# Kernel tuning notes

Hardware: AMD Instinct MI355X
Metric: run time of the kernel (lower is better)

The kernel has to match this reference:

```python
import jax, jax.numpy as jnp
import numpy as np

B, N, XS = 32, 200000, 256
SCALE = 100.0      # generator.scale_factor (grid-units per normalized coord)
CENTER = XS / 2.0  # xmipp_origin
W0_FIRST = 30.0    # SIREN first-layer frequency
SIGMA = 1.0        # gaussianFilterImage sigma
RAD = 3            # gaussian kernel radius (size 7)


def setup_inputs() -> dict:
    key = jax.random.key(0)
    ks = jax.random.split(key, 8)
    rows = jax.random.normal(ks[0], (B, 3), jnp.float32)            # euler angles (rad)
    shifts = jax.random.normal(ks[1], (B, 2), jnp.float32)          # in-plane shifts (px)
    coords = jax.random.uniform(ks[2], (N, 3), jnp.float32, -1.0, 1.0)  # point cloud in [-1,1]^3
    fan_in = 3 * N
    # SIRENFirstLayerInitializer(scale=6.0): U(-scale/fan_in, scale/fan_in)
    W1 = jax.random.uniform(ks[3], (fan_in, 8), jnp.float32, -6.0 / fan_in, 6.0 / fan_in)
    b1 = jnp.zeros((8,), jnp.float32)
    lim = float(np.sqrt(6.0 / 8.0))
    Wh = jax.random.uniform(ks[4], (3, 8, 8), jnp.float32, -lim, lim)
    bh = jnp.zeros((3, 8), jnp.float32)
    W5 = jax.random.normal(ks[5], (8, N), jnp.float32) * 0.05
    b5 = jnp.zeros((N,), jnp.float32)
    ctf = jax.random.uniform(ks[6], (B, XS, XS // 2 + 1), jnp.float32)  # rfft2 CTF filter
    return dict(rows=rows, shifts=shifts, coords=coords, W1=W1, b1=b1,
                Wh=Wh, bh=bh, W5=W5, b5=b5, ctf=ctf)


def euler_zyz(angles):
    # ZYZ Euler rotation matrices, (B,3,3)
    a, b, g = angles[:, 0], angles[:, 1], angles[:, 2]
    def rz(t):
        c, s = jnp.cos(t), jnp.sin(t)
        z, o = jnp.zeros_like(t), jnp.ones_like(t)
        return jnp.stack([jnp.stack([c, -s, z], -1),
                          jnp.stack([s, c, z], -1),
                          jnp.stack([z, z, o], -1)], -2)
    def ry(t):
        c, s = jnp.cos(t), jnp.sin(t)
        z, o = jnp.zeros_like(t), jnp.ones_like(t)
        return jnp.stack([jnp.stack([c, z, s], -1),
                          jnp.stack([z, o, z], -1),
                          jnp.stack([-s, z, c], -1)], -2)
    return rz(a) @ ry(b) @ rz(g)


def reference(rows, shifts, coords, W1, b1, Wh, bh, W5, b5, ctf):
    # --- getRotatedGrid: rotate fixed point cloud by per-image Euler angles ---
    R = euler_zyz(rows)                                   # (B,3,3)
    crot = jnp.einsum('bij,nj->bni', R, coords)           # (B,N,3)
    # --- SIREN MLP on flattened grid (Concatenate+Flatten -> Dense(8) stack) ---
    h = jnp.sin(W0_FIRST * (crot.reshape(B, 3 * N) @ W1 + b1))  # (B,8)
    for i in range(3):
        h = jnp.sin(h @ Wh[i] + bh[i])
    delta = h @ W5 + b5                                   # (B,N) per-point intensities
    # --- scatterImgByPass: bilinear scatter of intensities into (B,XS,XS) ---
    pos = crot[:, :, :2] * SCALE + CENTER - shifts[:, None, :]   # (B,N,2) -> (x,y) px
    x, y = pos[..., 0], pos[..., 1]
    x0 = jnp.floor(x); y0 = jnp.floor(y)
    fx = x - x0; fy = y - y0
    x0i = x0.astype(jnp.int32); y0i = y0.astype(jnp.int32)
    img = jnp.zeros((B, XS, XS), jnp.float32)
    bidx = jnp.arange(B, dtype=jnp.int32)[:, None]
    corners = ((0, 0, (1 - fx) * (1 - fy)), (1, 0, fx * (1 - fy)),
               (0, 1, (1 - fx) * fy), (1, 1, fx * fy))
    for dx, dy, w in corners:
        xi = x0i + dx; yi = y0i + dy
        valid = (xi >= 0) & (xi < XS) & (yi >= 0) & (yi < XS)
        xi = jnp.clip(xi, 0, XS - 1); yi = jnp.clip(yi, 0, XS - 1)
        img = img.at[bidx, yi, xi].add(jnp.where(valid, w * delta, 0.0))
    # --- gaussianFilterImage: separable gaussian blur, sigma=1 ---
    k = jnp.exp(-0.5 * (jnp.arange(-RAD, RAD + 1, dtype=jnp.float32) / SIGMA) ** 2)
    k = k / k.sum()
    dn = ('NCHW', 'OIHW', 'NCHW')
    x4 = img[:, None]                                     # (B,1,XS,XS)
    x4 = jax.lax.conv_general_dilated(x4, k.reshape(1, 1, 2 * RAD + 1, 1),
                                      (1, 1), 'SAME', dimension_numbers=dn)
    x4 = jax.lax.conv_general_dilated(x4, k.reshape(1, 1, 1, 2 * RAD + 1),
                                      (1, 1), 'SAME', dimension_numbers=dn)
    img = x4[:, 0]
    # --- ctfFilterImage: multiply by CTF in Fourier space ---
    F = jnp.fft.rfft2(img)
    out = jnp.fft.irfft2(F * ctf, s=(XS, XS))
    return out.astype(jnp.float32)
```

## Files before the change

kernel.cpp:

```cpp
#include <hip/hip_runtime.h>
#include <math.h>

constexpr int B_  = 32;
constexpr int N_  = 200000;
constexpr int XSZ = 256;
constexpr int PADS = 257;

constexpr int NQ = 4;
constexpr int BQ = 8;
constexpr int NSLAB = 32;
constexpr int BINS_Q = BQ * NSLAB;
constexpr int FILLB = 256;
constexpr int PPB = 782;
constexpr unsigned ENT_N = 1600000;

constexpr float FP_SCALE = 4194304.f;
constexpr float FP_INV   = 1.f / 4194304.f;

constexpr size_t OFF_PART  = 0;
constexpr size_t OFF_H     = 73728;
constexpr size_t OFF_R     = 74752;
constexpr size_t OFF_CNT   = 76800;
constexpr size_t OFF_INTRA = OFF_CNT + 524288;
constexpr size_t OFF_TOT   = OFF_INTRA + 1048576;
constexpr size_t OFF_BB    = OFF_TOT + 4096;
constexpr size_t OFF_APR   = OFF_BB + 4096;
constexpr size_t OFF_IMG   = OFF_APR + 1048576;
constexpr size_t OFF_ENT   = OFF_IMG + 8388608;
constexpr size_t OFF_TMP   = OFF_ENT;
constexpr size_t OFF_FC    = OFF_ENT;

__device__ __forceinline__ int rev8(int x) { return (int)(__brev((unsigned)x) >> 24); }

__device__ __forceinline__ void projPxPy(float c0, float c1, float c2,
                                         const float* sRb, const float* ssb,
                                         float& px, float& py) {
  px = fmaf(sRb[0], c0, fmaf(sRb[1], c1, fmaf(sRb[2], c2, ssb[0])));
  py = fmaf(sRb[3], c0, fmaf(sRb[4], c1, fmaf(sRb[5], c2, ssb[1])));
}

__global__ __launch_bounds__(256) void k_reduceT(const float* __restrict__ coords,
                                                 const float* __restrict__ W1,
                                                 float* __restrict__ partial) {
  float acc[72];
  #pragma unroll
  for (int t = 0; t < 72; ++t) acc[t] = 0.f;
  int idx = blockIdx.x * 256 + threadIdx.x;
  for (int n = idx; n < N_; n += 256 * 256) {
    float c0 = coords[n * 3 + 0], c1 = coords[n * 3 + 1], c2 = coords[n * 3 + 2];
    const float4* w4 = reinterpret_cast<const float4*>(W1 + (size_t)n * 24);
    #pragma unroll
    for (int i = 0; i < 3; ++i) {
      float4 wa = w4[i * 2 + 0], wb = w4[i * 2 + 1];
      float wv[8] = {wa.x, wa.y, wa.z, wa.w, wb.x, wb.y, wb.z, wb.w};
      #pragma unroll
      for (int k = 0; k < 8; ++k) {
        acc[i * 8 + k]      += c0 * wv[k];
        acc[24 + i * 8 + k] += c1 * wv[k];
        acc[48 + i * 8 + k] += c2 * wv[k];
      }
    }
  }
  #pragma unroll
  for (int t = 0; t < 72; ++t) {
    float v = acc[t];
    for (int off = 32; off > 0; off >>= 1) v += __shfl_down(v, off, 64);
    acc[t] = v;
  }
  __shared__ float sred[4][72];
  int lane = threadIdx.x & 63, wv_ = threadIdx.x >> 6;
  if (lane == 0) {
    #pragma unroll
    for (int t = 0; t < 72; ++t) sred[wv_][t] = acc[t];
  }
  __syncthreads();
  if (threadIdx.x < 72) {
    int t = threadIdx.x;
    partial[blockIdx.x * 72 + t] = sred[0][t] + sred[1][t] + sred[2][t] + sred[3][t];
  }
}

__global__ __launch_bounds__(128) void k_batch(const float* __restrict__ partial,
                                               const float* __restrict__ rows,
                                               const float* __restrict__ b1,
                                               const float* __restrict__ Wh,
                                               const float* __restrict__ bh,
                                               float* __restrict__ hbuf,
                                               float* __restrict__ Rbuf) {
  __shared__ float T[72];
  int tid = threadIdx.x;
  if (tid < 72) {
    double s = 0.0;
    for (int i = 0; i < 256; ++i) s += (double)partial[i * 72 + tid];
    T[tid] = (float)s;
  }
  __syncthreads();
  if (tid < B_) {
    int b = tid;
    float al = rows[b * 3 + 0], be = rows[b * 3 + 1], ga = rows[b * 3 + 2];
    float sa, ca, sb, cb, sg, cg;
    sincosf(al, &sa, &ca); sincosf(be, &sb, &cb); sincosf(ga, &sg, &cg);
    float R[3][3];
    R[0][0] = ca * cb * cg - sa * sg; R[0][1] = -ca * cb * sg - sa * cg; R[0][2] = ca * sb;
    R[1][0] = sa * cb * cg + ca * sg; R[1][1] = -sa * cb * sg + ca * cg; R[1][2] = sa * sb;
    R[2][0] = -sb * cg;               R[2][1] = sb * sg;                 R[2][2] = cb;
    float h[8];
    #pragma unroll
    for (int k = 0; k < 8; ++k) {
      float z = b1[k];
      #pragma unroll
      for (int i = 0; i < 3; ++i)
        #pragma unroll
        for (int j = 0; j < 3; ++j)
          z += R[i][j] * T[(j * 3 + i) * 8 + k];
      h[k] = sinf(30.f * z);
    }
    for (int l = 0; l < 3; ++l) {
      float nh[8];
      #pragma unroll
      for (int k2 = 0; k2 < 8; ++k2) {
        float z = bh[l * 8 + k2];
        #pragma unroll
        for (int k1 = 0; k1 < 8; ++k1) z += h[k1] * Wh[l * 64 + k1 * 8 + k2];
        nh[k2] = sinf(z);
      }
      #pragma unroll
      for (int k = 0; k < 8; ++k) h[k] = nh[k];
    }
    #pragma unroll
    for (int k = 0; k < 8; ++k) hbuf[b * 8 + k] = h[k];
    #pragma unroll
    for (int i = 0; i < 3; ++i)
      #pragma unroll
      for (int j = 0; j < 3; ++j) Rbuf[b * 9 + i * 3 + j] = R[i][j];
  }
}

__global__ __launch_bounds__(512) void k_count(const float* __restrict__ coords,
                                               const float* __restrict__ Rbuf,
                                               const float* __restrict__ shifts,
                                               unsigned short* __restrict__ cnt) {
  __shared__ float sR[BQ][6];
  __shared__ float ss[BQ][2];
  __shared__ unsigned hist[BINS_Q];
  int tid = threadIdx.x;
  int q = blockIdx.x >> 8;
  int fb = blockIdx.x & 255;
  if (tid < BQ) {
    int b = q * BQ + tid;
    sR[tid][0] = Rbuf[b * 9 + 0] * 100.f; sR[tid][1] = Rbuf[b * 9 + 1] * 100.f; sR[tid][2] = Rbuf[b * 9 + 2] * 100.f;
    sR[tid][3] = Rbuf[b * 9 + 3] * 100.f; sR[tid][4] = Rbuf[b * 9 + 4] * 100.f; sR[tid][5] = Rbuf[b * 9 + 5] * 100.f;
    ss[tid][0] = 128.f - shifts[b * 2 + 0];
    ss[tid][1] = 128.f - shifts[b * 2 + 1];
  }
  if (tid < BINS_Q) hist[tid] = 0;
  __syncthreads();
  int pbase = fb * PPB;
  #pragma unroll
  for (int k = 0; k < 2; ++k) {
    int off = tid + (k << 9);
    int n = pbase + off;
    if (off < PPB && n < N_) {
      float c0 = coords[n * 3], c1 = coords[n * 3 + 1], c2 = coords[n * 3 + 2];
      #pragma unroll
      for (int b = 0; b < BQ; ++b) {
        float px, py;
        projPxPy(c0, c1, c2, sR[b], ss[b], px, py);
        if (px >= -1.f && px < 256.f && py >= -1.f && py < 256.f) {
          int y0 = (int)floorf(py);
          int slab = (y0 < 0 ? 0 : y0) >> 3;
          atomicAdd(&hist[b * NSLAB + slab], 1u);
        }
      }
    }
  }
  __syncthreads();
  if (tid < BINS_Q) cnt[(size_t)blockIdx.x * BINS_Q + tid] = (unsigned short)hist[tid];
}

__global__ __launch_bounds__(256) void k_offA(const unsigned short* __restrict__ cnt,
                                              unsigned* __restrict__ intra,
                                              unsigned* __restrict__ totals) {
  int q = blockIdx.x >> 8;
  int bin = blockIdx.x & 255;
  int t = threadIdx.x;
  size_t cbase = ((size_t)q * FILLB + t) * BINS_Q + bin;
  unsigned orig = cnt[cbase];
  unsigned v = orig;
  int lane = t & 63, wid = t >> 6;
  #pragma unroll
  for (int d = 1; d < 64; d <<= 1) { unsigned u = __shfl_up(v, d, 64); if (lane >= d) v += u; }
  __shared__ unsigned wsum[4];
  if (lane == 63) wsum[wid] = v;
  __syncthreads();
  unsigned woff = 0;
  #pragma unroll
  for (int w = 0; w < 4; ++w) if (w < wid) woff += wsum[w];
  intra[cbase] = woff + v - orig;
  if (t == 255) totals[q * BINS_Q + bin] = woff + v;
}

__global__ __launch_bounds__(256) void k_offB(const unsigned* __restrict__ totals,
                                              unsigned* __restrict__ binBase) {
  int q = blockIdx.x;
  int t = threadIdx.x;
  unsigned orig = totals[q * BINS_Q + t];
  unsigned v = orig;
  int lane = t & 63, wid = t >> 6;
  #pragma unroll
  for (int d = 1; d < 64; d <<= 1) { unsigned u = __shfl_up(v, d, 64); if (lane >= d) v += u; }
  __shared__ unsigned wsum[4];
  if (lane == 63) wsum[wid] = v;
  __syncthreads();
  unsigned woff = 0;
  #pragma unroll
  for (int w = 0; w < 4; ++w) if (w < wid) woff += wsum[w];
  binBase[q * BINS_Q + t] = woff + v - orig;
}

__global__ __launch_bounds__(512) void k_fill2(const float* __restrict__ coords,
                                               const float* __restrict__ W5,
                                               const float* __restrict__ b5,
                                               const float* __restrict__ hbuf,
                                               const float* __restrict__ Rbuf,
                                               const float* __restrict__ shifts,
                                               const unsigned* __restrict__ intra,
                                               const unsigned* __restrict__ binBase,
                                               float2* __restrict__ ent) {
  __shared__ float sR[BQ][6];
  __shared__ float ss[BQ][2];
  __shared__ float sh[BQ][8];
  __shared__ unsigned scur[BINS_Q];
  int tid = threadIdx.x;
  int q = blockIdx.x >> 8;
  int fb = blockIdx.x & 255;
  if (tid < BQ) {
    int b = q * BQ + tid;
    sR[tid][0] = Rbuf[b * 9 + 0] * 100.f; sR[tid][1] = Rbuf[b * 9 + 1] * 100.f; sR[tid][2] = Rbuf[b * 9 + 2] * 100.f;
    sR[tid][3] = Rbuf[b * 9 + 3] * 100.f; sR[tid][4] = Rbuf[b * 9 + 4] * 100.f; sR[tid][5] = Rbuf[b * 9 + 5] * 100.f;
    ss[tid][0] = 128.f - shifts[b * 2 + 0];
    ss[tid][1] = 128.f - shifts[b * 2 + 1];
    #pragma unroll
    for (int k = 0; k < 8; ++k) sh[tid][k] = hbuf[b * 8 + k];
  }
  if (tid < BINS_Q)
    scur[tid] = binBase[q * BINS_Q + tid] + intra[((size_t)q * FILLB + fb) * BINS_Q + tid];
  __syncthreads();
  float2* entq = ent + (size_t)q * ENT_N;
  int pbase = fb * PPB;
  #pragma unroll
  for (int k = 0; k < 2; ++k) {
    int off = tid + (k << 9);
    int n = pbase + off;
    if (off < PPB && n < N_) {
      float c0 = coords[n * 3], c1 = coords[n * 3 + 1], c2 = coords[n * 3 + 2];
      float b5n = b5[n];
      float w5v[8];
      #pragma unroll
      for (int kk = 0; kk < 8; ++kk) w5v[kk] = W5[(size_t)kk * N_ + n];
      #pragma unroll
      for (int b = 0; b < BQ; ++b) {
        float px, py;
        projPxPy(c0, c1, c2, sR[b], ss[b], px, py);
        if (px >= -1.f && px < 256.f && py >= -1.f && py < 256.f) {
          int y0 = (int)floorf(py);
          int slab = (y0 < 0 ? 0 : y0) >> 3;
          int bin = b * NSLAB + slab;
          unsigned slot = atomicAdd(&scur[bin], 1u);
          if (slot < ENT_N) {
            float delta = b5n;
            #pragma unroll
            for (int kk = 0; kk < 8; ++kk) delta = fmaf(sh[b][kk], w5v[kk], delta);
            entq[slot] = make_float2(__int_as_float(n), delta);
          }
        }
      }
    }
  }
}

__global__ __launch_bounds__(512) void k_scatter2(const float2* __restrict__ ent,
                                                  const float* __restrict__ coords,
                                                  const float* __restrict__ Rbuf,
                                                  const float* __restrict__ shifts,
                                                  const unsigned* __restrict__ binBase,
                                                  const unsigned* __restrict__ totals,
                                                  float* __restrict__ img,
                                                  float* __restrict__ apron) {
  __shared__ int tile[9 * XSZ];
  __shared__ float sA[8];
  int tid = threadIdx.x;
  int q = blockIdx.x >> 8;
  int bin = blockIdx.x & 255;
  int b_local = bin >> 5;
  int s = bin & 31;
  int b_global = q * BQ + b_local;
  if (tid < 6)      sA[tid] = Rbuf[b_global * 9 + tid] * 100.f;
  else if (tid < 8) sA[tid] = 128.f - shifts[b_global * 2 + (tid - 6)];
  for (int i = tid; i < 9 * XSZ; i += 512) tile[i] = 0;
  __syncthreads();
  unsigned base = binBase[q * BINS_Q + bin];
  unsigned cntv = totals[q * BINS_Q + bin];
  if (base >= ENT_N) cntv = 0;
  else if (base + cntv > ENT_N) cntv = ENT_N - base;
  const float2* entq = ent + (size_t)q * ENT_N;
  int ybase = s << 3;
  for (unsigned i = tid; i < cntv; i += 512) {
    float2 e = entq[base + i];
    int n = __float_as_int(e.x);
    float delta = e.y;
    float c0 = coords[n * 3], c1 = coords[n * 3 + 1], c2 = coords[n * 3 + 2];
    float px, py;
    projPxPy(c0, c1, c2, sA, sA + 6, px, py);
    float x0f = floorf(px), y0f = floorf(py);
    float fx = px - x0f, fy = py - y0f;
    int x0 = (int)x0f;
    int r0 = (int)y0f - ybase;
    float wy0 = (1.f - fy) * delta * FP_SCALE;
    float wy1 = fy * delta * FP_SCALE;
    bool xl = (x0 >= 0), xr = (x0 <= 254);
    if (r0 >= 0) {
      int c0i = r0 * XSZ + x0;
      if (xl) atomicAdd(&tile[c0i], __float2int_rn((1.f - fx) * wy0));
      if (xr) atomicAdd(&tile[c0i + 1], __float2int_rn(fx * wy0));
    }
    int c1i = (r0 + 1) * XSZ + x0;
    if (xl) atomicAdd(&tile[c1i], __float2int_rn((1.f - fx) * wy1));
    if (xr) atomicAdd(&tile[c1i + 1], __float2int_rn(fx * wy1));
  }
  __syncthreads();
  float* imbase = img + (size_t)b_global * 65536 + (size_t)ybase * XSZ;
  for (int i = tid; i < 8 * XSZ; i += 512) imbase[i] = (float)tile[i] * FP_INV;
  if (tid < XSZ) apron[(size_t)(q * BINS_Q + bin) * XSZ + tid] = (float)tile[8 * XSZ + tid] * FP_INV;
}

__global__ __launch_bounds__(256) void k_apron(const float* __restrict__ apron,
                                               float* __restrict__ img) {
  int bid = blockIdx.x;
  int s = bid & 31;
  if (s == 31) return;
  int b = bid >> 5;
  int q = b >> 3, b_local = b & 7;
  int bin = b_local * NSLAB + s;
  int row = (s + 1) << 3;
  float* dst = img + (size_t)b * 65536 + (size_t)row * XSZ;
  dst[threadIdx.x] += apron[(size_t)(q * BINS_Q + bin) * XSZ + threadIdx.x];
}

__device__ __forceinline__ float bwv(int i) {
  const float bw[7] = {0.004433048f, 0.054005582f, 0.242036226f, 0.399050280f,
                       0.242036226f, 0.054005582f, 0.004433048f};
  return bw[i];
}

__global__ __launch_bounds__(256) void k_blurV(const float* __restrict__ in, float* __restrict__ out) {
  int i = blockIdx.x * 256 + threadIdx.x;
  int x = i & 255;
  int y = (i >> 8) & 255;
  const float* p = in + (i & ~65535);
  float s = 0.f;
  #pragma unroll
  for (int d = -3; d <= 3; ++d) {
    int yy = y + d;
    if ((unsigned)yy < XSZ) s += bwv(d + 3) * p[(yy << 8) + x];
  }
  out[i] = s;
}

__global__ __launch_bounds__(256) void k_blurH(const float* __restrict__ in, float* __restrict__ out) {
  int i = blockIdx.x * 256 + threadIdx.x;
  int x = i & 255;
  float s = 0.f;
  #pragma unroll
  for (int d = -3; d <= 3; ++d) {
    int xx = x + d;
    if ((unsigned)xx < XSZ) s += bwv(d + 3) * in[i + d];
  }
  out[i] = s;
}

__device__ __forceinline__ void fft_dif_fwd(float* re, float* im, const float2* tw, int P, int tid) {
  for (int s = 7; s >= 0; --s) {
    __syncthreads();
    int half = 1 << s;
    for (int q = tid; q < (P << 7); q += 256) {
      int p = q >> 7, k = q & 127;
      int j = k & (half - 1);
      int i0 = ((k >> s) << (s + 1)) | j;
      int i1 = i0 + half;
      float* rp = re + p * PADS; float* ip = im + p * PADS;
      float ar = rp[i0], ai = ip[i0], br = rp[i1], bi = ip[i1];
      rp[i0] = ar + br; ip[i0] = ai + bi;
      float tr = ar - br, ti = ai - bi;
      float2 w = tw[j << (7 - s)];
      rp[i1] = tr * w.x - ti * w.y;
      ip[i1] = tr * w.y + ti * w.x;
    }
  }
  __syncthreads();
}

__device__ __forceinline__ void fft_dit_inv(float* re, float* im, const float2* tw, int P, int tid) {
  for (int s = 0; s <= 7; ++s) {
    __syncthreads();
    int half = 1 << s;
    for (int q = tid; q < (P << 7); q += 256) {
      int p = q >> 7, k = q & 127;
      int j = k & (half - 1);
      int i0 = ((k >> s) << (s + 1)) | j;
      int i1 = i0 + half;
      float* rp = re + p * PADS; float* ip = im + p * PADS;
      float2 w = tw[j << (7 - s)];
      float br = rp[i1], bi = ip[i1];
      float tr = br * w.x + bi * w.y;
      float ti = bi * w.x - br * w.y;
      float ar = rp[i0], ai = ip[i0];
      rp[i0] = ar + tr; ip[i0] = ai + ti;
      rp[i1] = ar - tr; ip[i1] = ai - ti;
    }
  }
  __syncthreads();
}

__device__ __forceinline__ void tw_init(float2* tw, int tid) {
  for (int k = tid; k < 128; k += 256) {
    float s_, c_;
    sincosf(-6.2831853071795864769f * (float)k / 256.0f, &s_, &c_);
    tw[k] = make_float2(c_, s_);
  }
}

__global__ __launch_bounds__(256) void k_fft1(const float* __restrict__ img, float2* __restrict__ Fc) {
  __shared__ float re[16 * PADS], im[16 * PADS];
  __shared__ float2 tw[128];
  int tid = threadIdx.x;
  int b = blockIdx.x >> 4;
  int y0 = (blockIdx.x & 15) << 4;
  tw_init(tw, tid);
  const float* src = img + (size_t)b * 65536 + (size_t)y0 * 256;
  for (int q = tid; q < 4096; q += 256) {
    int j = q >> 8, x = q & 255;
    re[j * PADS + x] = src[j * 256 + x];
    im[j * PADS + x] = 0.f;
  }
  fft_dif_fwd(re, im, tw, 16, tid);
  float2* dst = Fc + (size_t)b * 65536;
  for (int q = tid; q < 4096; q += 256) {
    int j = q & 15, i = q >> 4;
    dst[(size_t)i * 256 + y0 + j] = make_float2(re[j * PADS + i], im[j * PADS + i]);
  }
}

__global__ __launch_bounds__(256) void k_fft2(float2* __restrict__ Fc, const float* __restrict__ ctf) {
  __shared__ float re[4 * PADS], im[4 * PADS];
  __shared__ float2 tw[128];
  int tid = threadIdx.x;
  int b = blockIdx.x >> 6;
  int r0 = (blockIdx.x & 63) << 2;
  tw_init(tw, tid);
  float2* base = Fc + (size_t)b * 65536 + (size_t)r0 * 256;
  for (int q = tid; q < 1024; q += 256) {
    int p = q >> 8, y = q & 255;
    float2 v = base[p * 256 + y];
    re[p * PADS + y] = v.x; im[p * PADS + y] = v.y;
  }
  fft_dif_fwd(re, im, tw, 4, tid);
  for (int q = tid; q < 1024; q += 256) {
    int p = q >> 8, iy = q & 255;
    int kx = rev8(r0 + p), ky = rev8(iy);
    float c;
    if (kx <= 128) c = ctf[((size_t)b * 256 + ky) * 129 + kx];
    else           c = ctf[((size_t)b * 256 + ((256 - ky) & 255)) * 129 + (256 - kx)];
    re[p * PADS + iy] *= c; im[p * PADS + iy] *= c;
  }
  fft_dit_inv(re, im, tw, 4, tid);
  for (int q = tid; q < 1024; q += 256) {
    int p = q >> 8, y = q & 255;
    base[p * 256 + y] = make_float2(re[p * PADS + y], im[p * PADS + y]);
  }
}

__global__ __launch_bounds__(256) void k_fft3(const float2* __restrict__ Fc, float* __restrict__ out) {
  __shared__ float re[16 * PADS], im[16 * PADS];
  __shared__ float2 tw[128];
  int tid = threadIdx.x;
  int b = blockIdx.x >> 4;
  int y0 = (blockIdx.x & 15) << 4;
  tw_init(tw, tid);
  const float2* src = Fc + (size_t)b * 65536;
  for (int q = tid; q < 4096; q += 256) {
    int j = q & 15, r = q >> 4;
    float2 v = src[(size_t)r * 256 + y0 + j];
    re[j * PADS + r] = v.x; im[j * PADS + r] = v.y;
  }
  fft_dit_inv(re, im, tw, 16, tid);
  float* dst = out + (size_t)b * 65536 + (size_t)y0 * 256;
  for (int q = tid; q < 4096; q += 256) {
    int j = q >> 8, x = q & 255;
    dst[j * 256 + x] = re[j * PADS + x] * (1.f / 65536.f);
  }
}

extern "C" void kernel_launch(void* const* d_in, const int* in_sizes, int n_in,
                              void* d_out, int out_size, void* d_ws, size_t ws_size,
                              hipStream_t stream) {
  const float* rows   = (const float*)d_in[0];
  const float* shifts = (const float*)d_in[1];
  const float* coords = (const float*)d_in[2];
  const float* W1     = (const float*)d_in[3];
  const float* b1     = (const float*)d_in[4];
  const float* Wh     = (const float*)d_in[5];
  const float* bh     = (const float*)d_in[6];
  const float* W5     = (const float*)d_in[7];
  const float* b5     = (const float*)d_in[8];
  const float* ctf    = (const float*)d_in[9];
  float* out = (float*)d_out;
  char* ws = (char*)d_ws;

  float*          partial = (float*)(ws + OFF_PART);
  float*          hbuf    = (float*)(ws + OFF_H);
  float*          Rbuf    = (float*)(ws + OFF_R);
  unsigned short* cnt     = (unsigned short*)(ws + OFF_CNT);
  unsigned*       intra   = (unsigned*)(ws + OFF_INTRA);
  unsigned*       totals  = (unsigned*)(ws + OFF_TOT);
  unsigned*       binBase = (unsigned*)(ws + OFF_BB);
  float*          apron   = (float*)(ws + OFF_APR);
  float*          img     = (float*)(ws + OFF_IMG);
  float2*         ent     = (float2*)(ws + OFF_ENT);
  float*          tmp     = (float*)(ws + OFF_TMP);
  float2*         Fc      = (float2*)(ws + OFF_FC);

  k_reduceT<<<256, 256, 0, stream>>>(coords, W1, partial);
  k_batch<<<1, 128, 0, stream>>>(partial, rows, b1, Wh, bh, hbuf, Rbuf);
  k_count<<<NQ * FILLB, 512, 0, stream>>>(coords, Rbuf, shifts, cnt);
  k_offA<<<NQ * BINS_Q, 256, 0, stream>>>(cnt, intra, totals);
  k_offB<<<NQ, 256, 0, stream>>>(totals, binBase);
  k_fill2<<<NQ * FILLB, 512, 0, stream>>>(coords, W5, b5, hbuf, Rbuf, shifts,
                                          intra, binBase, ent);
  k_scatter2<<<NQ * BINS_Q, 512, 0, stream>>>(ent, coords, Rbuf, shifts,
                                              binBase, totals, img, apron);
  k_apron<<<B_ * NSLAB, 256, 0, stream>>>(apron, img);
  k_blurV<<<B_ * XSZ * XSZ / 256, 256, 0, stream>>>(img, tmp);
  k_blurH<<<B_ * XSZ * XSZ / 256, 256, 0, stream>>>(tmp, img);
  k_fft1<<<B_ * 16, 256, 0, stream>>>(img, Fc);
  k_fft2<<<B_ * 64, 256, 0, stream>>>(Fc, ctf);
  k_fft3<<<B_ * 16, 256, 0, stream>>>(Fc, out);
}
```

Before: 179.6 us.

## Fuse separable Gaussian blur into first FFT pass and unroll scatter loop

The vertical and horizontal blur kernels are removed. The first row-FFT kernel now loads a 22-row band with a 3-row halo into shared memory, applies both blur passes there, and then runs the FFT, which removes two full-image global round trips and two launches. Separately, the scatter loop handles two entries per thread per iteration so that entry and coordinate loads overlap. The shared-memory footprint of the FFT kernel grows, which may lower occupancy, and the halo rows are reloaded redundantly across blocks.

New measurement: 166.9 us, median of 2. 7.0% less time.

```diff
diff --git a/kernel.cpp b/kernel.cpp
--- a/kernel.cpp
+++ b/kernel.cpp
@@ -27,7 +27,6 @@
 constexpr size_t OFF_APR   = OFF_BB + 4096;
 constexpr size_t OFF_IMG   = OFF_APR + 1048576;
 constexpr size_t OFF_ENT   = OFF_IMG + 8388608;
-constexpr size_t OFF_TMP   = OFF_ENT;
 constexpr size_t OFF_FC    = OFF_ENT;
 
 __device__ __forceinline__ int rev8(int x) { return (int)(__brev((unsigned)x) >> 24); }
@@ -305,11 +304,8 @@
   else if (base + cntv > ENT_N) cntv = ENT_N - base;
   const float2* entq = ent + (size_t)q * ENT_N;
   int ybase = s << 3;
-  for (unsigned i = tid; i < cntv; i += 512) {
-    float2 e = entq[base + i];
-    int n = __float_as_int(e.x);
-    float delta = e.y;
-    float c0 = coords[n * 3], c1 = coords[n * 3 + 1], c2 = coords[n * 3 + 2];
+
+  auto doEntry = [&](float c0, float c1, float c2, float delta) {
     float px, py;
     projPxPy(c0, c1, c2, sA, sA + 6, px, py);
     float x0f = floorf(px), y0f = floorf(py);
@@ -327,6 +323,22 @@
     int c1i = (r0 + 1) * XSZ + x0;
     if (xl) atomicAdd(&tile[c1i], __float2int_rn((1.f - fx) * wy1));
     if (xr) atomicAdd(&tile[c1i + 1], __float2int_rn(fx * wy1));
+  };
+
+  for (unsigned i = tid; i < cntv; i += 1024) {
+    unsigned i1 = i + 512;
+    bool v1 = i1 < cntv;
+    float2 e0 = entq[base + i];
+    float2 e1 = v1 ? entq[base + i1] : make_float2(0.f, 0.f);
+    int n0 = __float_as_int(e0.x);
+    float c00 = coords[n0 * 3], c01 = coords[n0 * 3 + 1], c02 = coords[n0 * 3 + 2];
+    float c10 = 0.f, c11 = 0.f, c12 = 0.f;
+    if (v1) {
+      int n1 = __float_as_int(e1.x);
+      c10 = coords[n1 * 3]; c11 = coords[n1 * 3 + 1]; c12 = coords[n1 * 3 + 2];
+    }
+    doEntry(c00, c01, c02, e0.y);
+    if (v1) doEntry(c10, c11, c12, e1.y);
   }
   __syncthreads();
   float* imbase = img + (size_t)b_global * 65536 + (size_t)ybase * XSZ;
@@ -351,32 +363,6 @@
   const float bw[7] = {0.004433048f, 0.054005582f, 0.242036226f, 0.399050280f,
                        0.242036226f, 0.054005582f, 0.004433048f};
   return bw[i];
-}
-
-__global__ __launch_bounds__(256) void k_blurV(const float* __restrict__ in, float* __restrict__ out) {
-  int i = blockIdx.x * 256 + threadIdx.x;
-  int x = i & 255;
-  int y = (i >> 8) & 255;
-  const float* p = in + (i & ~65535);
-  float s = 0.f;
-  #pragma unroll
-  for (int d = -3; d <= 3; ++d) {
-    int yy = y + d;
-    if ((unsigned)yy < XSZ) s += bwv(d + 3) * p[(yy << 8) + x];
-  }
-  out[i] = s;
-}
-
-__global__ __launch_bounds__(256) void k_blurH(const float* __restrict__ in, float* __restrict__ out) {
-  int i = blockIdx.x * 256 + threadIdx.x;
-  int x = i & 255;
-  float s = 0.f;
-  #pragma unroll
-  for (int d = -3; d <= 3; ++d) {
-    int xx = x + d;
-    if ((unsigned)xx < XSZ) s += bwv(d + 3) * in[i + d];
-  }
-  out[i] = s;
 }
 
 __device__ __forceinline__ void fft_dif_fwd(float* re, float* im, const float2* tw, int P, int tid) {
@@ -430,18 +416,42 @@
   }
 }
 
-__global__ __launch_bounds__(256) void k_fft1(const float* __restrict__ img, float2* __restrict__ Fc) {
-  __shared__ float re[16 * PADS], im[16 * PADS];
+__global__ __launch_bounds__(256) void k_fft1b(const float* __restrict__ img, float2* __restrict__ Fc) {
+  __shared__ float smem[13840];
   __shared__ float2 tw[128];
+  float* raw = smem;
+  float* bv  = smem + 5632;
+  float* re  = smem;
+  float* im  = smem + 9728;
   int tid = threadIdx.x;
   int b = blockIdx.x >> 4;
   int y0 = (blockIdx.x & 15) << 4;
   tw_init(tw, tid);
-  const float* src = img + (size_t)b * 65536 + (size_t)y0 * 256;
+  const float* src = img + (size_t)b * 65536;
+  for (int q = tid; q < 22 * 256; q += 256) {
+    int j = q >> 8, x = q & 255;
+    int y = y0 - 3 + j;
+    raw[q] = ((unsigned)y < 256u) ? src[y * 256 + x] : 0.f;
+  }
+  __syncthreads();
   for (int q = tid; q < 4096; q += 256) {
-    int j = q >> 8, x = q & 255;
-    re[j * PADS + x] = src[j * 256 + x];
-    im[j * PADS + x] = 0.f;
+    int r = q >> 8, x = q & 255;
+    float s = 0.f;
+    #pragma unroll
+    for (int d = 0; d < 7; ++d) s += bwv(d) * raw[(r + d) * 256 + x];
+    bv[q] = s;
+  }
+  __syncthreads();
+  for (int q = tid; q < 4096; q += 256) {
+    int r = q >> 8, x = q & 255;
+    float s = 0.f;
+    #pragma unroll
+    for (int e = -3; e <= 3; ++e) {
+      int xx = x + e;
+      if ((unsigned)xx < 256u) s += bwv(e + 3) * bv[r * 256 + xx];
+    }
+    re[r * PADS + x] = s;
+    im[r * PADS + x] = 0.f;
   }
   fft_dif_fwd(re, im, tw, 16, tid);
   float2* dst = Fc + (size_t)b * 65536;
@@ -527,7 +537,6 @@
   float*          apron   = (float*)(ws + OFF_APR);
   float*          img     = (float*)(ws + OFF_IMG);
   float2*         ent     = (float2*)(ws + OFF_ENT);
-  float*          tmp     = (float*)(ws + OFF_TMP);
   float2*         Fc      = (float2*)(ws + OFF_FC);
 
   k_reduceT<<<256, 256, 0, stream>>>(coords, W1, partial);
@@ -540,9 +549,7 @@
   k_scatter2<<<NQ * BINS_Q, 512, 0, stream>>>(ent, coords, Rbuf, shifts,
                                               binBase, totals, img, apron);
   k_apron<<<B_ * NSLAB, 256, 0, stream>>>(apron, img);
-  k_blurV<<<B_ * XSZ * XSZ / 256, 256, 0, stream>>>(img, tmp);
-  k_blurH<<<B_ * XSZ * XSZ / 256, 256, 0, stream>>>(tmp, img);
-  k_fft1<<<B_ * 16, 256, 0, stream>>>(img, Fc);
+  k_fft1b<<<B_ * 16, 256, 0, stream>>>(img, Fc);
   k_fft2<<<B_ * 64, 256, 0, stream>>>(Fc, ctf);
   k_fft3<<<B_ * 16, 256, 0, stream>>>(Fc, out);
 }
```
